# Performance work log

Measured on AMD Instinct MI355X. Metric: run time of the kernel, lower is better.

The kernel has to match this reference:

```python
import jax, jax.numpy as jnp
import numpy as np
import math

D_MODEL = 2048
HEADS = 16
D_K = D_MODEL // HEADS
B, S = 4, 2048


def setup_inputs() -> dict:
    key = jax.random.key(0)
    ks = jax.random.split(key, 11)
    scale = 1.0 / math.sqrt(D_MODEL)
    inp = {
        "q": jax.random.normal(ks[0], (B, S, D_MODEL), dtype=jnp.float32),
        "k": jax.random.normal(ks[1], (B, S, D_MODEL), dtype=jnp.float32),
        "v": jax.random.normal(ks[2], (B, S, D_MODEL), dtype=jnp.float32),
        "w_q": jax.random.normal(ks[3], (D_MODEL, D_MODEL), dtype=jnp.float32) * scale,
        "b_q": jnp.zeros((D_MODEL,), dtype=jnp.float32),
        "w_k": jax.random.normal(ks[4], (D_MODEL, D_MODEL), dtype=jnp.float32) * scale,
        "b_k": jnp.zeros((D_MODEL,), dtype=jnp.float32),
        "w_v": jax.random.normal(ks[5], (D_MODEL, D_MODEL), dtype=jnp.float32) * scale,
        "b_v": jnp.zeros((D_MODEL,), dtype=jnp.float32),
        "w_o": jax.random.normal(ks[6], (D_MODEL, D_MODEL), dtype=jnp.float32) * scale,
        "b_o": jnp.zeros((D_MODEL,), dtype=jnp.float32),
    }
    return inp


def reference(q, k, v, w_q, b_q, w_k, b_k, w_v, b_v, w_o, b_o):
    # Linear projections (torch Linear: x @ W^T + b; here W stored pre-transposed)
    query = q @ w_q + b_q  # [B,S,D]
    key = k @ w_k + b_k
    value = v @ w_v + b_v
    # split heads -> [B,H,S,d_k]
    def split(x):
        return x.reshape(B, S, HEADS, D_K).transpose(0, 2, 1, 3)
    qh, kh, vh = split(query), split(key), split(value)
    # scaled dot-product attention (full score matrix, as in original)
    scores = jnp.einsum('bhqd,bhkd->bhqk', qh, kh) / jnp.sqrt(jnp.float32(D_K))
    attn = jax.nn.softmax(scores, axis=-1)
    out = jnp.einsum('bhqk,bhkd->bhqd', attn, vh)  # [B,H,S,d_k]
    out = out.transpose(0, 2, 1, 3).reshape(B, S, D_MODEL)
    return out @ w_o + b_o
```

## Files before the change

kernel.cpp:

```cpp
#include <hip/hip_runtime.h>
#include <hip/hip_bf16.h>

#define DMODEL 2048
#define HEADS 16
#define DK 128
#define BATCH 4
#define SEQ 2048
#define MROWS (BATCH * SEQ)

typedef __attribute__((ext_vector_type(8))) short bf16x8;
typedef __attribute__((ext_vector_type(4))) short bf16x4;
typedef __attribute__((ext_vector_type(4))) float f32x4;
typedef __attribute__((ext_vector_type(16))) float f32x16;

static __device__ __forceinline__ short f2bf(float x) {
    __hip_bfloat16 h = __float2bfloat16(x);
    union { __hip_bfloat16 h; short s; } u;
    u.h = h;
    return u.s;
}

static __device__ __forceinline__ int cvt_pk_bf16(float lo, float hi) {
    int r;
    asm("v_cvt_pk_bf16_f32 %0, %1, %2" : "=v"(r) : "v"(lo), "v"(hi));
    return r;
}

static __device__ __forceinline__ float exp2_fast(float x) {
    float r;
    asm("v_exp_f32 %0, %1" : "=v"(r) : "v"(x));
    return r;
}

#define MFMA16(a, b, c) __builtin_amdgcn_mfma_f32_16x16x32_bf16((a), (b), (c), 0, 0, 0)
#define MFMA32(a, b, c) __builtin_amdgcn_mfma_f32_32x32x16_bf16((a), (b), (c), 0, 0, 0)

static __device__ __forceinline__ void load_lds16(const void* g, void* l) {
    __builtin_amdgcn_global_load_lds(
        (const __attribute__((address_space(1))) unsigned int*)g,
        (__attribute__((address_space(3))) unsigned int*)l, 16, 0, 0);
}

__global__ __launch_bounds__(256) void cvt3_bf16(
    const float* __restrict__ i0, const float* __restrict__ i1,
    const float* __restrict__ i2, short* __restrict__ o0,
    short* __restrict__ o1, short* __restrict__ o2, int n8) {
    int i = blockIdx.x * blockDim.x + threadIdx.x;
    const int stride = gridDim.x * blockDim.x;
    for (; i < 3 * n8; i += stride) {
        const int which = i / n8;
        const int idx = i - which * n8;
        const float* in = which == 0 ? i0 : (which == 1 ? i1 : i2);
        short* out = which == 0 ? o0 : (which == 1 ? o1 : o2);
        f32x4 a = ((const f32x4*)in)[idx * 2];
        f32x4 b = ((const f32x4*)in)[idx * 2 + 1];
        bf16x8 o;
        o[0] = f2bf(a[0]); o[1] = f2bf(a[1]); o[2] = f2bf(a[2]); o[3] = f2bf(a[3]);
        o[4] = f2bf(b[0]); o[5] = f2bf(b[1]); o[6] = f2bf(b[2]); o[7] = f2bf(b[3]);
        ((bf16x8*)out)[idx] = o;
    }
}

__global__ __launch_bounds__(256) void cvt_tr4(
    const float* __restrict__ w0, const float* __restrict__ w1,
    const float* __restrict__ w2, const float* __restrict__ w3,
    short* __restrict__ t0, short* __restrict__ t1,
    short* __restrict__ t2, short* __restrict__ t3) {
    __shared__ short t[64][72];
    const int which = blockIdx.z;
    const float* W = which == 0 ? w0 : (which == 1 ? w1 : (which == 2 ? w2 : w3));
    short* Wt = which == 0 ? t0 : (which == 1 ? t1 : (which == 2 ? t2 : t3));
    const int n0 = blockIdx.x * 64, k0 = blockIdx.y * 64;
    const int tid = threadIdx.x;
#pragma unroll
    for (int p = 0; p < 4; p++) {
        const int kr = p * 16 + (tid >> 4);
        const int nc = (tid & 15) * 4;
        f32x4 v = *(const f32x4*)&W[(size_t)(k0 + kr) * DMODEL + n0 + nc];
#pragma unroll
        for (int j = 0; j < 4; j++) t[nc + j][kr] = f2bf(v[j]);
    }
    __syncthreads();
    const int nr = tid >> 2, ch = (tid & 3) * 16;
    *(bf16x8*)&Wt[(size_t)(n0 + nr) * DMODEL + k0 + ch] = *(const bf16x8*)&t[nr][ch];
    *(bf16x8*)&Wt[(size_t)(n0 + nr) * DMODEL + k0 + ch + 8] = *(const bf16x8*)&t[nr][ch + 8];
}

__global__ __launch_bounds__(256) void tr_bf16(const short* __restrict__ in,
                                               short* __restrict__ out) {
    __shared__ short t[64][65];
    const int c0 = blockIdx.x * 64, r0 = blockIdx.y * 64;
    const int tid = threadIdx.x;
    const int row = tid >> 2, cb = (tid & 3) * 16;
    bf16x8 a = *(const bf16x8*)&in[(size_t)(r0 + row) * DMODEL + c0 + cb];
    bf16x8 b2 = *(const bf16x8*)&in[(size_t)(r0 + row) * DMODEL + c0 + cb + 8];
#pragma unroll
    for (int j = 0; j < 8; j++) { t[cb + j][row] = a[j]; t[cb + 8 + j][row] = b2[j]; }
    __syncthreads();
#pragma unroll
    for (int j = 0; j < 16; j++)
        out[(size_t)(c0 + row) * MROWS + r0 + cb + j] = t[row][cb + j];
}

static __device__ __forceinline__ void stageAu(const char* g, char* lds,
                                               int ro, int ktb, int tid, int wid) {
#pragma unroll
    for (int j = 0; j < 2; j++) {
        const int u = j * 64 + (tid >> 3);
        const int r = ((u & 63) | ((u >> 6) << 7)) + ro;
        const int rbase = wid * 8 + j * 128 + ro;
        load_lds16(g + (size_t)r * (DMODEL * 2) + ktb + (((tid & 7) * 16) ^ ((r & 7) << 4)),
                   lds + rbase * 128);
    }
}

static __device__ __forceinline__ void stageBu(const char* g, char* lds,
                                               int ro, int ktb, int tid, int wid) {
#pragma unroll
    for (int j = 0; j < 2; j++) {
        const int u = j * 64 + (tid >> 3);
        const int r = ((u & 31) | ((u >> 5) << 6)) + ro;
        const int rbase = (wid & 3) * 8 + (j * 2 + (wid >> 2)) * 64 + ro;
        load_lds16(g + (size_t)r * (DMODEL * 2) + ktb + (((tid & 7) * 16) ^ ((r & 7) << 4)),
                   lds + rbase * 128);
    }
}

#define PHASE_TOP(VMS)                                        \
    asm volatile("s_waitcnt lgkmcnt(0)" ::: "memory");        \
    asm volatile("s_waitcnt " VMS ::: "memory");              \
    __builtin_amdgcn_s_barrier();                             \
    __builtin_amdgcn_sched_barrier(0);

#define LOAD_AF(buf, mh)                                                          \
    _Pragma("unroll") for (int mi = 0; mi < 4; mi++)                              \
    _Pragma("unroll") for (int kk = 0; kk < 2; kk++)                              \
        af[mi][kk] = *(const bf16x8*)((const char*)Asl[buf] +                     \
            (wm * 128 + (mh) * 64 + mi * 16 + l15) * 128 + ((kk * 64 + fg) ^ fx));

#define LOAD_BF(dst, buf, nh)                                                     \
    _Pragma("unroll") for (int ni = 0; ni < 2; ni++)                              \
    _Pragma("unroll") for (int kk = 0; kk < 2; kk++)                              \
        dst[ni][kk] = *(const bf16x8*)((const char*)Bsl[buf] +                    \
            (wn * 64 + (nh) * 32 + ni * 16 + l15) * 128 + ((kk * 64 + fg) ^ fx));

#define MFMA_QUAD(mh, nh, bsrc)                                                   \
    __builtin_amdgcn_s_setprio(1);                                                \
    _Pragma("unroll") for (int mi = 0; mi < 4; mi++)                              \
    _Pragma("unroll") for (int ni = 0; ni < 2; ni++)                              \
    _Pragma("unroll") for (int kk = 0; kk < 2; kk++)                              \
        acc[(mh) * 4 + mi][(nh) * 2 + ni] =                                       \
            MFMA16(af[mi][kk], bsrc[ni][kk], acc[(mh) * 4 + mi][(nh) * 2 + ni]);  \
    __builtin_amdgcn_s_setprio(0);

template <typename OT, bool TRANSV = false>
__global__ __launch_bounds__(512, 2) void gemm9(
    const short* __restrict__ A, const short* __restrict__ Bt,
    const float* __restrict__ bias, OT* __restrict__ C, float oscale) {
    __shared__ short Asl[2][256 * 64];
    __shared__ short Bsl[2][256 * 64];
    const int tid = threadIdx.x, lane = tid & 63, wid = tid >> 6;

    const int nwg = gridDim.x;
    const int bid = blockIdx.x;
    const int swz = (bid & 7) * (nwg >> 3) + (bid >> 3);
    const int bx = swz >> 5, by = swz & 31;
    const int row0 = by * 256, col0 = bx * 256;
    const int wm = wid >> 2, wn = wid & 3;

    const char* Ab = (const char*)A + (size_t)row0 * (DMODEL * 2);
    const char* Bb = (const char*)Bt + (size_t)col0 * (DMODEL * 2);

    const int l15 = lane & 15;
    const int fg = (lane >> 4) * 16;
    const int fx = (lane & 7) << 4;

    f32x4 acc[8][4] = {};
    bf16x8 af[4][2], bA[2][2], bB[2][2];

    stageAu(Ab, (char*)Asl[0], 0, 0, tid, wid);
    stageBu(Bb, (char*)Bsl[0], 0, 0, tid, wid);
    stageBu(Bb, (char*)Bsl[0], 32, 0, tid, wid);
    stageAu(Ab, (char*)Asl[0], 64, 0, tid, wid);
    stageAu(Ab, (char*)Asl[1], 0, 128, tid, wid);

    const int NIT = DMODEL / 128;
    for (int it = 0; it < NIT - 1; it++) {
        const int o1 = (2 * it + 1) * 128;
        const int e2 = (2 * it + 2) * 128;
        const int o2 = (2 * it + 3) * 128;

        PHASE_TOP("vmcnt(6)");
        LOAD_AF(0, 0); LOAD_BF(bA, 0, 0);
        stageBu(Bb, (char*)Bsl[1], 0, o1, tid, wid);
        MFMA_QUAD(0, 0, bA);

        PHASE_TOP("vmcnt(6)");
        LOAD_BF(bB, 0, 1);
        stageBu(Bb, (char*)Bsl[1], 32, o1, tid, wid);
        MFMA_QUAD(0, 1, bB);

        PHASE_TOP("vmcnt(6)");
        LOAD_AF(0, 1);
        stageAu(Ab, (char*)Asl[1], 64, o1, tid, wid);
        MFMA_QUAD(1, 1, bB);

        PHASE_TOP("vmcnt(6)");
        stageAu(Ab, (char*)Asl[0], 0, e2, tid, wid);
        MFMA_QUAD(1, 0, bA);

        PHASE_TOP("vmcnt(6)");
        LOAD_AF(1, 0); LOAD_BF(bA, 1, 0);
        stageBu(Bb, (char*)Bsl[0], 0, e2, tid, wid);
        MFMA_QUAD(0, 0, bA);

        PHASE_TOP("vmcnt(6)");
        LOAD_BF(bB, 1, 1);
        stageBu(Bb, (char*)Bsl[0], 32, e2, tid, wid);
        MFMA_QUAD(0, 1, bB);

        PHASE_TOP("vmcnt(6)");
        LOAD_AF(1, 1);
        stageAu(Ab, (char*)Asl[0], 64, e2, tid, wid);
        MFMA_QUAD(1, 1, bB);

        PHASE_TOP("vmcnt(6)");
        stageAu(Ab, (char*)Asl[1], 0, o2, tid, wid);
        MFMA_QUAD(1, 0, bA);
    }

    {
        const int o1 = (DMODEL / 64 - 1) * 128;

        PHASE_TOP("vmcnt(6)");
        LOAD_AF(0, 0); LOAD_BF(bA, 0, 0);
        stageBu(Bb, (char*)Bsl[1], 0, o1, tid, wid);
        MFMA_QUAD(0, 0, bA);

        PHASE_TOP("vmcnt(6)");
        LOAD_BF(bB, 0, 1);
        stageBu(Bb, (char*)Bsl[1], 32, o1, tid, wid);
        MFMA_QUAD(0, 1, bB);

        PHASE_TOP("vmcnt(6)");
        LOAD_AF(0, 1);
        stageAu(Ab, (char*)Asl[1], 64, o1, tid, wid);
        MFMA_QUAD(1, 1, bB);

        PHASE_TOP("vmcnt(6)");
        MFMA_QUAD(1, 0, bA);

        PHASE_TOP("vmcnt(4)");
        LOAD_AF(1, 0); LOAD_BF(bA, 1, 0);
        MFMA_QUAD(0, 0, bA);

        PHASE_TOP("vmcnt(2)");
        LOAD_BF(bB, 1, 1);
        MFMA_QUAD(0, 1, bB);

        PHASE_TOP("vmcnt(0)");
        LOAD_AF(1, 1);
        MFMA_QUAD(1, 1, bB);

        PHASE_TOP("vmcnt(0)");
        MFMA_QUAD(1, 0, bA);
    }

#pragma unroll
    for (int n = 0; n < 4; n++) {
        const int col = col0 + wn * 64 + n * 16 + l15;
        const float bz = bias[col];
#pragma unroll
        for (int m = 0; m < 8; m++) {
            const int row4 = row0 + wm * 128 + m * 16 + (lane >> 4) * 4;
            if constexpr (TRANSV) {
                bf16x4 tv;
#pragma unroll
                for (int j = 0; j < 4; j++) tv[j] = f2bf((acc[m][n][j] + bz) * oscale);
                *(bf16x4*)&C[(size_t)col * MROWS + row4] = tv;
            } else {
#pragma unroll
                for (int j = 0; j < 4; j++) {
                    const float v = (acc[m][n][j] + bz) * oscale;
                    if constexpr (sizeof(OT) == 2)
                        C[(size_t)(row4 + j) * DMODEL + col] = (OT)f2bf(v);
                    else
                        C[(size_t)(row4 + j) * DMODEL + col] = (OT)v;
                }
            }
        }
    }
}

template <typename AT, typename OT>
__global__ __launch_bounds__(256) void gemm_kernel(
    const AT* __restrict__ A, const float* __restrict__ W,
    const float* __restrict__ bias, OT* __restrict__ C, float oscale) {
    const int K = DMODEL, N = DMODEL;
    __shared__ short As[128][40];
    __shared__ short Bs[128][40];
    const int tid = threadIdx.x;
    const int lane = tid & 63;
    const int wid = tid >> 6;
    const int wm = wid >> 1, wn = wid & 1;
    const int row0 = blockIdx.y * 128;
    const int col0 = blockIdx.x * 128;
    f32x4 acc[4][4] = {};
    const int a_row = tid >> 1;
    const int a_col = (tid & 1) * 16;
    const int b_n = (tid & 31) * 4;
    const int b_k = (tid >> 5) * 4;
    for (int k0 = 0; k0 < K; k0 += 32) {
        __syncthreads();
        {
            const AT* src = A + (size_t)(row0 + a_row) * K + k0 + a_col;
            if constexpr (sizeof(AT) == 4) {
                const float* sf = reinterpret_cast<const float*>(src);
                f32x4 v0 = *(const f32x4*)(sf + 0);
                f32x4 v1 = *(const f32x4*)(sf + 4);
                f32x4 v2 = *(const f32x4*)(sf + 8);
                f32x4 v3 = *(const f32x4*)(sf + 12);
                bf16x8 w0, w1;
                w0[0] = f2bf(v0[0]); w0[1] = f2bf(v0[1]); w0[2] = f2bf(v0[2]); w0[3] = f2bf(v0[3]);
                w0[4] = f2bf(v1[0]); w0[5] = f2bf(v1[1]); w0[6] = f2bf(v1[2]); w0[7] = f2bf(v1[3]);
                w1[0] = f2bf(v2[0]); w1[1] = f2bf(v2[1]); w1[2] = f2bf(v2[2]); w1[3] = f2bf(v2[3]);
                w1[4] = f2bf(v3[0]); w1[5] = f2bf(v3[1]); w1[6] = f2bf(v3[2]); w1[7] = f2bf(v3[3]);
                *(bf16x8*)&As[a_row][a_col + 0] = w0;
                *(bf16x8*)&As[a_row][a_col + 8] = w1;
            } else {
                const short* ss = reinterpret_cast<const short*>(src);
                *(bf16x8*)&As[a_row][a_col + 0] = *(const bf16x8*)(ss + 0);
                *(bf16x8*)&As[a_row][a_col + 8] = *(const bf16x8*)(ss + 8);
            }
        }
        {
            const float* w0p = W + (size_t)(k0 + b_k + 0) * N + col0 + b_n;
            f32x4 r0 = *(const f32x4*)(w0p);
            f32x4 r1 = *(const f32x4*)(w0p + N);
            f32x4 r2 = *(const f32x4*)(w0p + 2 * N);
            f32x4 r3 = *(const f32x4*)(w0p + 3 * N);
#pragma unroll
            for (int j = 0; j < 4; j++) {
                bf16x4 t;
                t[0] = f2bf(r0[j]); t[1] = f2bf(r1[j]); t[2] = f2bf(r2[j]); t[3] = f2bf(r3[j]);
                *(bf16x4*)&Bs[b_n + j][b_k] = t;
            }
        }
        __syncthreads();
        bf16x8 af[4], bfr[4];
#pragma unroll
        for (int m = 0; m < 4; m++)
            af[m] = *(const bf16x8*)&As[wm * 64 + m * 16 + (lane & 15)][(lane >> 4) * 8];
#pragma unroll
        for (int n = 0; n < 4; n++)
            bfr[n] = *(const bf16x8*)&Bs[wn * 64 + n * 16 + (lane & 15)][(lane >> 4) * 8];
#pragma unroll
        for (int m = 0; m < 4; m++)
#pragma unroll
            for (int n = 0; n < 4; n++)
                acc[m][n] = MFMA16(af[m], bfr[n], acc[m][n]);
    }
#pragma unroll
    for (int m = 0; m < 4; m++) {
#pragma unroll
        for (int n = 0; n < 4; n++) {
            const int col = col0 + wn * 64 + n * 16 + (lane & 15);
            const float bz = bias[col];
#pragma unroll
            for (int j = 0; j < 4; j++) {
                const int row = row0 + wm * 64 + m * 16 + (lane >> 4) * 4 + j;
                const float v = (acc[m][n][j] + bz) * oscale;
                if constexpr (sizeof(OT) == 2)
                    C[(size_t)row * N + col] = (OT)f2bf(v);
                else
                    C[(size_t)row * N + col] = (OT)v;
            }
        }
    }
}

__global__ __launch_bounds__(512, 2) void attn_kernel(
    const short* __restrict__ Qp, const short* __restrict__ Kp,
    const short* __restrict__ Vtp, short* __restrict__ Oout) {
    const int nwg = gridDim.x;
    const int bid = blockIdx.x;
    const int bx = (bid & 7) * (nwg >> 3) + (bid >> 3);
    const int qt = bx & 7;
    const int h = (bx >> 3) & 15;
    const int b = bx >> 7;

    __shared__ short Ks[2][128 * 128];
    __shared__ short Vts[2][128 * 128];

    const int tid = threadIdx.x;
    const int lane = tid & 63;
    const int wid = tid >> 6;
    const int lo = lane & 31;
    const int hi1 = lane >> 5;

    bf16x8 qf[8];
    {
        const short* qrow = Qp + (size_t)(b * SEQ + qt * 256 + wid * 32 + lo) * DMODEL + h * DK;
#pragma unroll
        for (int dk = 0; dk < 8; dk++)
            qf[dk] = *(const bf16x8*)(qrow + dk * 16 + hi1 * 8);
    }

    f32x16 oacc[4] = {};
    float lsum = 0.f;

    const char* Kbase = (const char*)(Kp + (size_t)(b * SEQ) * DMODEL + h * DK);
    const char* Vtbase = (const char*)(Vtp + (size_t)(h * DK) * MROWS + b * SEQ);

    const int srow = wid * 16 + (lane >> 4);
    const int scp = (lane & 15) * 16;
    const int NT = SEQ / 128;
    const float C12 = 17.3123404906676f;

#pragma unroll
    for (int i = 0; i < 4; i++) {
        const int rr = srow + i * 4;
        load_lds16(Kbase + (size_t)rr * (DMODEL * 2) + (scp ^ ((rr & 15) << 4)),
                   (char*)Ks[0] + wid * 4096 + i * 1024);
    }
#pragma unroll
    for (int i = 0; i < 4; i++) {
        const int dd = srow + i * 4;
        load_lds16(Vtbase + (size_t)dd * (MROWS * 2) + (scp ^ ((dd & 15) << 4)),
                   (char*)Vts[0] + wid * 4096 + i * 1024);
    }
    asm volatile("s_waitcnt vmcnt(0)" ::: "memory");
    __builtin_amdgcn_s_barrier();
    __builtin_amdgcn_sched_barrier(0);

    for (int kt = 0; kt < NT; kt++) {
        const int cur = kt & 1;
        const bool more = (kt + 1) < NT;

        if (more) {
#pragma unroll
            for (int i = 0; i < 4; i++) {
                const int rr = srow + i * 4;
                load_lds16(Kbase + (size_t)((kt + 1) * 128 + rr) * (DMODEL * 2) + (scp ^ ((rr & 15) << 4)),
                           (char*)Ks[cur ^ 1] + wid * 4096 + i * 1024);
            }
#pragma unroll
            for (int i = 0; i < 4; i++) {
                const int dd = srow + i * 4;
                load_lds16(Vtbase + (size_t)dd * (MROWS * 2) + (kt + 1) * 256 + (scp ^ ((dd & 15) << 4)),
                           (char*)Vts[cur ^ 1] + wid * 4096 + i * 1024);
            }
        }

        f32x16 sc[2];
        bf16x8 pa[8];

        sc[0] = (f32x16){};
        __builtin_amdgcn_s_setprio(1);
#pragma unroll
        for (int dk = 0; dk < 8; dk++) {
            const int r = 0 * 32 + lo;
            const int cb = (dk * 32 + hi1 * 16) ^ ((r & 15) << 4);
            bf16x8 kf = *(const bf16x8*)((char*)Ks[cur] + r * 256 + cb);
            sc[0] = MFMA32(kf, qf[dk], sc[0]);
        }
        __builtin_amdgcn_s_setprio(0);

#pragma unroll
        for (int g = 0; g < 4; g++) {
            if (g < 3) {
                sc[(g + 1) & 1] = (f32x16){};
                __builtin_amdgcn_s_setprio(1);
#pragma unroll
                for (int dk = 0; dk < 8; dk++) {
                    const int r = (g + 1) * 32 + lo;
                    const int cb = (dk * 32 + hi1 * 16) ^ ((r & 15) << 4);
                    bf16x8 kf = *(const bf16x8*)((char*)Ks[cur] + r * 256 + cb);
                    sc[(g + 1) & 1] = MFMA32(kf, qf[dk], sc[(g + 1) & 1]);
                }
                __builtin_amdgcn_s_setprio(0);
            }
            {
                f32x16& s = sc[g & 1];
#pragma unroll
                for (int r = 0; r < 16; r++)
                    s[r] = exp2_fast(s[r] - C12);
                float s0 = 0.f, s1 = 0.f, s2 = 0.f, s3 = 0.f;
#pragma unroll
                for (int r = 0; r < 16; r += 4) {
                    s0 += s[r]; s1 += s[r + 1]; s2 += s[r + 2]; s3 += s[r + 3];
                }
                lsum += (s0 + s1) + (s2 + s3);
#pragma unroll
                for (int hf = 0; hf < 2; hf++) {
                    const int X0 = cvt_pk_bf16(s[8 * hf + 0], s[8 * hf + 1]);
                    const int X1 = cvt_pk_bf16(s[8 * hf + 2], s[8 * hf + 3]);
                    const int X2 = cvt_pk_bf16(s[8 * hf + 4], s[8 * hf + 5]);
                    const int X3 = cvt_pk_bf16(s[8 * hf + 6], s[8 * hf + 7]);
                    const int L0 = hi1 ? X2 : X0, L1 = hi1 ? X3 : X1;
                    const int S0 = hi1 ? X0 : X2, S1 = hi1 ? X1 : X3;
                    const int R0 = __shfl_xor(S0, 32, 64);
                    const int R1 = __shfl_xor(S1, 32, 64);
                    union { int i[4]; bf16x8 v; } u;
                    u.i[0] = hi1 ? R0 : L0;
                    u.i[1] = hi1 ? R1 : L1;
                    u.i[2] = hi1 ? L0 : R0;
                    u.i[3] = hi1 ? L1 : R1;
                    pa[2 * g + hf] = u.v;
                }
            }
        }

        __builtin_amdgcn_s_setprio(1);
#pragma unroll
        for (int ks = 0; ks < 8; ks++) {
#pragma unroll
            for (int n = 0; n < 4; n++) {
                const int d = n * 32 + lo;
                const int cb = (ks * 32 + hi1 * 16) ^ ((d & 15) << 4);
                bf16x8 vf = *(const bf16x8*)((char*)Vts[cur] + d * 256 + cb);
                oacc[n] = MFMA32(vf, pa[ks], oacc[n]);
            }
        }
        __builtin_amdgcn_s_setprio(0);

        if (more) {
            asm volatile("s_waitcnt vmcnt(0)" ::: "memory");
            asm volatile("s_waitcnt lgkmcnt(0)" ::: "memory");
            __builtin_amdgcn_s_barrier();
            __builtin_amdgcn_sched_barrier(0);
        }
    }

    const float l = lsum + __shfl_xor(lsum, 32, 64);
    const float inv = 1.0f / l;
    short* obase = Oout + (size_t)(b * SEQ + qt * 256 + wid * 32 + lo) * DMODEL + h * DK;
#pragma unroll
    for (int n = 0; n < 4; n++) {
#pragma unroll
        for (int rr = 0; rr < 8; rr++) {
            const int d = n * 32 + 2 * (rr & 1) + 8 * (rr >> 1) + 4 * hi1;
            const int pkv = cvt_pk_bf16(oacc[n][2 * rr] * inv, oacc[n][2 * rr + 1] * inv);
            *(int*)(obase + d) = pkv;
        }
    }
}

extern "C" void kernel_launch(void* const* d_in, const int* in_sizes, int n_in,
                              void* d_out, int out_size, void* d_ws, size_t ws_size,
                              hipStream_t stream) {
    const float* q   = (const float*)d_in[0];
    const float* k   = (const float*)d_in[1];
    const float* v   = (const float*)d_in[2];
    const float* w_q = (const float*)d_in[3];
    const float* b_q = (const float*)d_in[4];
    const float* w_k = (const float*)d_in[5];
    const float* b_k = (const float*)d_in[6];
    const float* w_v = (const float*)d_in[7];
    const float* b_v = (const float*)d_in[8];
    const float* w_o = (const float*)d_in[9];
    const float* b_o = (const float*)d_in[10];
    float* out = (float*)d_out;

    const size_t PROJ = (size_t)MROWS * DMODEL;
    const size_t WSZ = (size_t)DMODEL * DMODEL;
    const float qscale = 0.08838834764831845f * 1.4426950408889634f;
    const int attn_grid = BATCH * HEADS * (SEQ / 256);

    if (ws_size >= (6 * PROJ + 4 * WSZ) * sizeof(short)) {
        short* qbf = (short*)d_ws;
        short* kbf = qbf + PROJ;
        short* vbf = kbf + PROJ;
        short* Qp  = vbf + PROJ;
        short* Kp  = Qp + PROJ;
        short* Vt  = Kp + PROJ;
        short* wtq = Vt + PROJ;
        short* wtk = wtq + WSZ;
        short* wtv = wtk + WSZ;
        short* wto = wtv + WSZ;
        short* Ao  = qbf;

        const int n8 = (int)(PROJ / 8);
        cvt3_bf16<<<3072, 256, 0, stream>>>(q, k, v, qbf, kbf, vbf, n8);
        dim3 gtr(DMODEL / 64, DMODEL / 64, 4);
        cvt_tr4<<<gtr, 256, 0, stream>>>(w_q, w_k, w_v, w_o, wtq, wtk, wtv, wto);

        const int nwg8 = (MROWS / 256) * (DMODEL / 256);
        gemm9<short><<<nwg8, 512, 0, stream>>>(qbf, wtq, b_q, Qp, qscale);
        gemm9<short><<<nwg8, 512, 0, stream>>>(kbf, wtk, b_k, Kp, 1.0f);
        gemm9<short, true><<<nwg8, 512, 0, stream>>>(vbf, wtv, b_v, Vt, 1.0f);

        attn_kernel<<<attn_grid, 512, 0, stream>>>(Qp, Kp, Vt, Ao);

        gemm9<float><<<nwg8, 512, 0, stream>>>(Ao, wto, b_o, out, 1.0f);
    } else {
        short* Qp = (short*)d_ws;
        short* Kp = Qp + PROJ;
        short* Vp = Kp + PROJ;
        short* Vt = Vp + PROJ;
        short* Ao = Vt + PROJ;
        dim3 gblk(DMODEL / 128, MROWS / 128);
        gemm_kernel<float, short><<<gblk, 256, 0, stream>>>(q, w_q, b_q, Qp, qscale);
        gemm_kernel<float, short><<<gblk, 256, 0, stream>>>(k, w_k, b_k, Kp, 1.0f);
        gemm_kernel<float, short><<<gblk, 256, 0, stream>>>(v, w_v, b_v, Vp, 1.0f);
        dim3 gtrv(DMODEL / 64, MROWS / 64);
        tr_bf16<<<gtrv, 256, 0, stream>>>(Vp, Vt);
        attn_kernel<<<attn_grid, 512, 0, stream>>>(Qp, Kp, Vt, Ao);
        gemm_kernel<short, float><<<gblk, 256, 0, stream>>>(Ao, w_o, b_o, out, 1.0f);
    }
}
```

Before: 561.5 us.

## Restructure GEMM phase synchronization with split waits and double barriers

```diff
diff --git a/kernel.cpp b/kernel.cpp
--- a/kernel.cpp
+++ b/kernel.cpp
@@ -126,12 +126,6 @@
     }
 }
 
-#define PHASE_TOP(VMS)                                        \
-    asm volatile("s_waitcnt lgkmcnt(0)" ::: "memory");        \
-    asm volatile("s_waitcnt " VMS ::: "memory");              \
-    __builtin_amdgcn_s_barrier();                             \
-    __builtin_amdgcn_sched_barrier(0);
-
 #define LOAD_AF(buf, mh)                                                          \
     _Pragma("unroll") for (int mi = 0; mi < 4; mi++)                              \
     _Pragma("unroll") for (int kk = 0; kk < 2; kk++)                              \
@@ -153,8 +147,13 @@
             MFMA16(af[mi][kk], bsrc[ni][kk], acc[(mh) * 4 + mi][(nh) * 2 + ni]);  \
     __builtin_amdgcn_s_setprio(0);
 
+#define WAITV(N)  asm volatile("s_waitcnt vmcnt(" #N ")" ::: "memory")
+#define WAITL(N)  asm volatile("s_waitcnt lgkmcnt(" #N ")" ::: "memory")
+#define BARRIER() __builtin_amdgcn_s_barrier()
+#define SBAR()    __builtin_amdgcn_sched_barrier(0)
+
 template <typename OT, bool TRANSV = false>
-__global__ __launch_bounds__(512, 2) void gemm9(
+__global__ __launch_bounds__(512, 2) void gemm10(
     const short* __restrict__ A, const short* __restrict__ Bt,
     const float* __restrict__ bias, OT* __restrict__ C, float oscale) {
     __shared__ short Asl[2][256 * 64];
@@ -178,91 +177,124 @@
     f32x4 acc[8][4] = {};
     bf16x8 af[4][2], bA[2][2], bB[2][2];
 
-    stageAu(Ab, (char*)Asl[0], 0, 0, tid, wid);
-    stageBu(Bb, (char*)Bsl[0], 0, 0, tid, wid);
-    stageBu(Bb, (char*)Bsl[0], 32, 0, tid, wid);
-    stageAu(Ab, (char*)Asl[0], 64, 0, tid, wid);
-    stageAu(Ab, (char*)Asl[1], 0, 128, tid, wid);
+    char* As0 = (char*)Asl[0];
+    char* As1 = (char*)Asl[1];
+    char* Bs0 = (char*)Bsl[0];
+    char* Bs1 = (char*)Bsl[1];
+
+    stageAu(Ab, As0, 0, 0, tid, wid);
+    stageBu(Bb, Bs0, 0, 0, tid, wid);
+    stageBu(Bb, Bs0, 32, 0, tid, wid);
+    stageAu(Ab, As0, 64, 0, tid, wid);
+    stageAu(Ab, As1, 0, 128, tid, wid);
+    WAITV(6);
+    BARRIER();
+    SBAR();
 
     const int NIT = DMODEL / 128;
     for (int it = 0; it < NIT - 1; it++) {
-        const int o1 = (2 * it + 1) * 128;
-        const int e2 = (2 * it + 2) * 128;
-        const int o2 = (2 * it + 3) * 128;
-
-        PHASE_TOP("vmcnt(6)");
+        const int t1b = (2 * it + 1) * 128;
+        const int t2b = (2 * it + 2) * 128;
+        const int t3b = (2 * it + 3) * 128;
+
         LOAD_AF(0, 0); LOAD_BF(bA, 0, 0);
-        stageBu(Bb, (char*)Bsl[1], 0, o1, tid, wid);
+        stageBu(Bb, Bs1, 0, t1b, tid, wid);
+        WAITL(8); WAITV(6);
+        BARRIER(); WAITL(0); SBAR();
         MFMA_QUAD(0, 0, bA);
-
-        PHASE_TOP("vmcnt(6)");
+        BARRIER();
+
         LOAD_BF(bB, 0, 1);
-        stageBu(Bb, (char*)Bsl[1], 32, o1, tid, wid);
+        stageBu(Bb, Bs1, 32, t1b, tid, wid);
+        WAITV(6);
+        BARRIER(); WAITL(0); SBAR();
         MFMA_QUAD(0, 1, bB);
-
-        PHASE_TOP("vmcnt(6)");
+        BARRIER();
+
         LOAD_AF(0, 1);
-        stageAu(Ab, (char*)Asl[1], 64, o1, tid, wid);
+        stageAu(Ab, As1, 64, t1b, tid, wid);
+        BARRIER(); WAITL(0); SBAR();
         MFMA_QUAD(1, 1, bB);
-
-        PHASE_TOP("vmcnt(6)");
-        stageAu(Ab, (char*)Asl[0], 0, e2, tid, wid);
+        BARRIER();
+
+        stageAu(Ab, As0, 0, t2b, tid, wid);
+        WAITV(6);
+        BARRIER(); SBAR();
         MFMA_QUAD(1, 0, bA);
-
-        PHASE_TOP("vmcnt(6)");
+        BARRIER();
+
         LOAD_AF(1, 0); LOAD_BF(bA, 1, 0);
-        stageBu(Bb, (char*)Bsl[0], 0, e2, tid, wid);
+        stageBu(Bb, Bs0, 0, t2b, tid, wid);
+        WAITL(8); WAITV(6);
+        BARRIER(); WAITL(0); SBAR();
         MFMA_QUAD(0, 0, bA);
-
-        PHASE_TOP("vmcnt(6)");
+        BARRIER();
+
         LOAD_BF(bB, 1, 1);
-        stageBu(Bb, (char*)Bsl[0], 32, e2, tid, wid);
+        stageBu(Bb, Bs0, 32, t2b, tid, wid);
+        WAITV(6);
+        BARRIER(); WAITL(0); SBAR();
         MFMA_QUAD(0, 1, bB);
-
-        PHASE_TOP("vmcnt(6)");
+        BARRIER();
+
         LOAD_AF(1, 1);
-        stageAu(Ab, (char*)Asl[0], 64, e2, tid, wid);
+        stageAu(Ab, As0, 64, t2b, tid, wid);
+        BARRIER(); WAITL(0); SBAR();
         MFMA_QUAD(1, 1, bB);
-
-        PHASE_TOP("vmcnt(6)");
-        stageAu(Ab, (char*)Asl[1], 0, o2, tid, wid);
+        BARRIER();
+
+        stageAu(Ab, As1, 0, t3b, tid, wid);
+        WAITV(6);
+        BARRIER(); SBAR();
         MFMA_QUAD(1, 0, bA);
+        BARRIER();
     }
 
     {
-        const int o1 = (DMODEL / 64 - 1) * 128;
-
-        PHASE_TOP("vmcnt(6)");
+        const int t1b = (DMODEL / 64 - 1) * 128;
+
         LOAD_AF(0, 0); LOAD_BF(bA, 0, 0);
-        stageBu(Bb, (char*)Bsl[1], 0, o1, tid, wid);
+        stageBu(Bb, Bs1, 0, t1b, tid, wid);
+        WAITL(8); WAITV(6);
+        BARRIER(); WAITL(0); SBAR();
         MFMA_QUAD(0, 0, bA);
-
-        PHASE_TOP("vmcnt(6)");
+        BARRIER();
+
         LOAD_BF(bB, 0, 1);
-        stageBu(Bb, (char*)Bsl[1], 32, o1, tid, wid);
+        stageBu(Bb, Bs1, 32, t1b, tid, wid);
+        WAITV(6);
+        BARRIER(); WAITL(0); SBAR();
         MFMA_QUAD(0, 1, bB);
-
-        PHASE_TOP("vmcnt(6)");
+        BARRIER();
+
         LOAD_AF(0, 1);
-        stageAu(Ab, (char*)Asl[1], 64, o1, tid, wid);
+        stageAu(Ab, As1, 64, t1b, tid, wid);
+        BARRIER(); WAITL(0); SBAR();
         MFMA_QUAD(1, 1, bB);
-
-        PHASE_TOP("vmcnt(6)");
+        BARRIER();
+
+        WAITV(4);
+        BARRIER(); SBAR();
         MFMA_QUAD(1, 0, bA);
-
-        PHASE_TOP("vmcnt(4)");
+        BARRIER();
+
         LOAD_AF(1, 0); LOAD_BF(bA, 1, 0);
+        WAITL(8); WAITV(2);
+        BARRIER(); WAITL(0); SBAR();
         MFMA_QUAD(0, 0, bA);
-
-        PHASE_TOP("vmcnt(2)");
+        BARRIER();
+
         LOAD_BF(bB, 1, 1);
+        WAITV(0);
+        BARRIER(); WAITL(0); SBAR();
         MFMA_QUAD(0, 1, bB);
-
-        PHASE_TOP("vmcnt(0)");
+        BARRIER();
+
         LOAD_AF(1, 1);
+        BARRIER(); WAITL(0); SBAR();
         MFMA_QUAD(1, 1, bB);
-
-        PHASE_TOP("vmcnt(0)");
+        BARRIER();
+
         MFMA_QUAD(1, 0, bA);
     }
 
@@ -586,13 +618,13 @@
         cvt_tr4<<<gtr, 256, 0, stream>>>(w_q, w_k, w_v, w_o, wtq, wtk, wtv, wto);
 
         const int nwg8 = (MROWS / 256) * (DMODEL / 256);
-        gemm9<short><<<nwg8, 512, 0, stream>>>(qbf, wtq, b_q, Qp, qscale);
-        gemm9<short><<<nwg8, 512, 0, stream>>>(kbf, wtk, b_k, Kp, 1.0f);
-        gemm9<short, true><<<nwg8, 512, 0, stream>>>(vbf, wtv, b_v, Vt, 1.0f);
+        gemm10<short><<<nwg8, 512, 0, stream>>>(qbf, wtq, b_q, Qp, qscale);
+        gemm10<short><<<nwg8, 512, 0, stream>>>(kbf, wtk, b_k, Kp, 1.0f);
+        gemm10<short, true><<<nwg8, 512, 0, stream>>>(vbf, wtv, b_v, Vt, 1.0f);
 
         attn_kernel<<<attn_grid, 512, 0, stream>>>(Qp, Kp, Vt, Ao);
 
-        gemm9<float><<<nwg8, 512, 0, stream>>>(Ao, wto, b_o, out, 1.0f);
+        gemm10<float><<<nwg8, 512, 0, stream>>>(Ao, wto, b_o, out, 1.0f);
     } else {
         short* Qp = (short*)d_ws;
         short* Kp = Qp + PROJ;
```

After: 574.5 us. 1.02x slower.
